# Performance work log

Measured on AMD Instinct MI355X. Metric: run time of the kernel, lower is better.

## Reference

```python
import jax, jax.numpy as jnp
import numpy as np

WS = 5    # window_size
NH = 8    # num_heads
C = 96    # channels
LOG_MAX = float(np.log(1.0 / 0.01))  # clamp max for logit scales


def _conv3x3(x, w, b):
    # NCHW conv, stride 1, padding 1 ('SAME' for 3x3)
    y = jax.lax.conv_general_dilated(x, w, window_strides=(1, 1), padding='SAME',
                                     dimension_numbers=('NCHW', 'OIHW', 'NCHW'))
    return y + b[None, :, None, None]


def _l2norm(x):
    # matches F.normalize(dim=-1): x / max(||x||, 1e-12)
    n = jnp.linalg.norm(x, axis=-1, keepdims=True)
    return x / jnp.maximum(n, 1e-12)


def _wa(f, x, logit_scale):
    # f: (b, c, h, w); x: (b, 2c, h, w) -> windowed cosine attention
    b, c2, h, w = x.shape
    c = f.shape[1]
    hd = c // NH
    H, W = h // WS, w // WS
    # q: b (nh hd) (H ws) (W ws) -> (b H W) nh (ws ws) hd
    q = f.reshape(b, NH, hd, H, WS, W, WS).transpose(0, 3, 5, 1, 4, 6, 2)
    q = q.reshape(b * H * W, NH, WS * WS, hd)
    kv = x.reshape(b, 2, NH, hd, H, WS, W, WS).transpose(1, 0, 4, 6, 2, 5, 7, 3)
    kv = kv.reshape(2, b * H * W, NH, WS * WS, hd)
    k, v = kv[0], kv[1]
    scale = jnp.exp(jnp.minimum(logit_scale, LOG_MAX))  # (NH,1,1)
    atn = jnp.einsum('wnic,wnjc->wnij', _l2norm(q), _l2norm(k)) * scale[None]
    atn = jax.nn.softmax(atn, axis=-1)
    y = jnp.einsum('wnij,wnjc->wnic', atn, v)
    # back to (b, nh*hd, h, w)
    y = y.reshape(b, H, W, NH, WS, WS, hd).transpose(0, 3, 6, 1, 4, 2, 5)
    return y.reshape(b, c, h, w)


def reference(x, w_in, b_in, w_f, b_f, w_out, b_out, logit_scale, lr_logit_scale):
    b, c, h, w = x.shape
    xp = _conv3x3(x, w_in, b_in)   # (b, 2c, h, w)
    fp = _conv3x3(x, w_f, b_f)     # (b, c, h, w)
    sc2, sc = 2 * c // 3, c // 3
    xs = [xp[:, i * sc2:(i + 1) * sc2] for i in range(3)]
    fs = [fp[:, i * sc:(i + 1) * sc] for i in range(3)]
    ys = []
    # branch 0: plain window attention
    ys.append(_wa(fs[0], xs[0], logit_scale))
    # branch 1: shifted windows (torch rolls by -WS//2 = -3 and restores +WS//2 = +2)
    sh = -WS // 2  # Python: (-5)//2 = -3, matches torch code
    x_ = jnp.roll(xs[1], (sh, sh), axis=(2, 3))
    f_ = jnp.roll(fs[1], (sh, sh), axis=(2, 3))
    y_ = _wa(f_, x_, logit_scale)
    ys.append(jnp.roll(y_, (WS // 2, WS // 2), axis=(2, 3)))
    # branch 2: long-range axial (row then column) cosine attention
    hd = sc // NH
    q = fs[2].reshape(b, NH, hd, h, w).transpose(0, 1, 3, 4, 2)            # (b,n,h,w,c)
    kv = xs[2].reshape(b, 2, NH, hd, h, w).transpose(1, 0, 2, 4, 5, 3)      # (2,b,n,h,w,c)
    k, v = kv[0], kv[1]
    qn, kn = _l2norm(q), _l2norm(k)
    scale = jnp.exp(jnp.minimum(lr_logit_scale, LOG_MAX)).reshape(1, NH, 1, 1, 1)
    # row attention (over w)
    atn = jnp.einsum('bnhic,bnhjc->bnhij', qn, kn) * scale
    atn = jax.nn.softmax(atn, axis=-1)
    v = jnp.einsum('bnhij,bnhjc->bnhic', atn, v)
    # column attention (over h), reusing normalized q/k and same scale
    atn = jnp.einsum('bniwc,bnjwc->bnwij', qn, kn) * scale
    atn = jax.nn.softmax(atn, axis=-1)
    v = jnp.einsum('bnwij,bnjwc->bniwc', atn, v)
    ys.append(v.transpose(0, 1, 4, 2, 3).reshape(b, sc, h, w))
    y = jnp.concatenate(ys, axis=1)  # (b, c, h, w)
    return _conv3x3(y, w_out, b_out)


def setup_inputs() -> dict:
    key = jax.random.key(0)
    ks = jax.random.split(key, 8)
    B, H, W = 1, 240, 240
    inp = {
        'x': jax.random.normal(ks[0], (B, C, H, W), dtype=jnp.float32),
        'w_in': jax.random.normal(ks[1], (2 * C, C, 3, 3), dtype=jnp.float32) * 0.03,
        'b_in': jax.random.normal(ks[2], (2 * C,), dtype=jnp.float32) * 0.01,
        'w_f': jax.random.normal(ks[3], (C, C, 3, 3), dtype=jnp.float32) * 0.03,
        'b_f': jax.random.normal(ks[4], (C,), dtype=jnp.float32) * 0.01,
        'w_out': jax.random.normal(ks[5], (C, C, 3, 3), dtype=jnp.float32) * 0.03,
        'b_out': jax.random.normal(ks[6], (C,), dtype=jnp.float32) * 0.01,
        'logit_scale': jnp.log(10.0) * jnp.ones((NH, 1, 1), dtype=jnp.float32),
        'lr_logit_scale': jnp.log(10.0) * jnp.ones((NH, 1, 1), dtype=jnp.float32),
    }
    return inp
```

## Files before the change

### kernel.cpp

```cpp
#include <hip/hip_runtime.h>
#include <math.h>

#define HH 240
#define WW 240
#define PP (HH * WW)
#define PW 242
#define LOG_MAX_C 4.605170185988091f
#define LOG2E 1.442695040888963f

typedef __bf16 bf16x8 __attribute__((ext_vector_type(8)));
typedef float  f32x4  __attribute__((ext_vector_type(4)));

#define EXP2F(x) __builtin_amdgcn_exp2f(x)


__device__ __forceinline__ void to_xs_pad_body(
    int p, const float* __restrict__ in, __bf16* __restrict__ xs)
{
    if (p >= PW * PW) return;
    const int row = p / PW, px = p % PW;
    const bool border = (row == 0 || row == PW - 1 || px == 0 || px == PW - 1);
    union { __bf16 h[32]; uint4 u[4]; } pk;
#pragma unroll
    for (int icb = 0; icb < 3; ++icb) {
        uint4* op = (uint4*)(xs + (((size_t)row * 3 + icb) * PW + px) * 32);
        if (border) {
#pragma unroll
            for (int b = 0; b < 4; ++b) op[b] = make_uint4(0, 0, 0, 0);
        } else {
            const float* ip = in + (size_t)(icb * 32) * PP + (row - 1) * WW + (px - 1);
#pragma unroll
            for (int j = 0; j < 32; ++j) pk.h[j] = (__bf16)ip[(size_t)j * PP];
#pragma unroll
            for (int b = 0; b < 4; ++b) op[b] = pk.u[b];
        }
    }
}

__device__ __forceinline__ void wt_frag_body(
    int t, const float* __restrict__ w, __bf16* __restrict__ wtf, int OC)
{
    if (t >= 9 * (OC / 16) * 3 * 64) return;
    const int lane = t & 63;
    const int rest = t >> 6;
    const int icb  = rest % 3;
    const int to   = rest / 3;
    const int ocb  = to % (OC / 16);
    const int tap  = to / (OC / 16);
    const int ln = lane & 15, quad = lane >> 4;
    const int oc  = ocb * 16 + ln;
    const int ic0 = icb * 32 + quad * 8;
    __bf16* op = wtf + (size_t)rest * 512 + lane * 8;
#pragma unroll
    for (int d = 0; d < 8; ++d)
        op[d] = (__bf16)w[(size_t)(oc * 96 + ic0 + d) * 9 + tap];
}

__global__ __launch_bounds__(256) void prep_kernel(
    const float* __restrict__ x, const float* __restrict__ w_in,
    const float* __restrict__ w_f, const float* __restrict__ w_out,
    __bf16* __restrict__ xs, __bf16* __restrict__ wtf_in,
    __bf16* __restrict__ wtf_f, __bf16* __restrict__ wtf_o)
{
    const int bid = blockIdx.x, tid = threadIdx.x;
    if (bid < 81)       wt_frag_body(bid * 256 + tid, w_in, wtf_in, 192);
    else if (bid < 122) wt_frag_body((bid - 81) * 256 + tid, w_f, wtf_f, 96);
    else if (bid < 163) wt_frag_body((bid - 122) * 256 + tid, w_out, wtf_o, 96);
    else                to_xs_pad_body((bid - 163) * 256 + tid, x, xs);
}

template <int OC, int MT, int EPI>
__device__ __forceinline__ void conv_body(
    int bid, const __bf16* __restrict__ xs, const __bf16* __restrict__ wtf,
    const float* __restrict__ bias, float* __restrict__ out0,
    float* __restrict__ out1, const float* __restrict__ lsc,
    const float* __restrict__ lrlsc, __bf16* As)
{
    const int group = bid / 24;
    const int w24   = bid % 24;
    const int z     = w24 >> 3;
    const int xy    = group * 8 + (w24 & 7);
    if (xy >= 450) return;
    const int x0  = (xy % 15) * 16;
    const int y0  = (xy / 15) * 8;
    const int oc0 = z * (MT * 16);
    const int ocb0 = oc0 / 16;

    const int wave = threadIdx.x >> 6;
    const int lane = threadIdx.x & 63;
    const int ln   = lane & 15;
    const int quad = lane >> 4;
    const int r0   = y0 + wave * 2;

    f32x4 acc[MT][2] = {};
    bf16x8 a[MT], b[2][2], astg;

    const __bf16* abase = wtf + (size_t)lane * 8;
    const __bf16* bbase = xs + (size_t)ln * 32 + quad * 8;

#define ASRC(c) (abase + ((size_t)(((c) / 3) * (OC / 16) + ocb0 + wave) * 3 + (c) % 3) * 512)
#define BLOAD(c, buf)                                                         \
    {                                                                         \
        const int tap_ = (c) / 3, icb_ = (c) % 3;                             \
        const int dy_ = tap_ / 3, dx_ = tap_ % 3;                             \
        _Pragma("unroll")                                                     \
        for (int ni = 0; ni < 2; ++ni)                                        \
            b[buf][ni] = *(const bf16x8*)(bbase +                             \
                (((size_t)(r0 + ni + dy_) * 3 + icb_) * PW + x0 + dx_) * 32); \
    }

    if (wave < MT) {
        astg = *(const bf16x8*)ASRC(0);
        *(bf16x8*)(As + (size_t)wave * 512 + lane * 8) = astg;
        astg = *(const bf16x8*)ASRC(1);
    }
    BLOAD(0, 0)

#pragma unroll
    for (int c = 0; c < 27; ++c) {
        const int cur = c & 1, nxt = cur ^ 1;
        __syncthreads();
        if (c < 26 && wave < MT)
            *(bf16x8*)(As + ((size_t)(nxt * MT) + wave) * 512 + lane * 8) = astg;
#pragma unroll
        for (int mi = 0; mi < MT; ++mi)
            a[mi] = *(const bf16x8*)(As + ((size_t)(cur * MT) + mi) * 512 + lane * 8);
        if (c < 25 && wave < MT)
            astg = *(const bf16x8*)ASRC(c + 2);
        if (c < 26) BLOAD(c + 1, nxt)
#pragma unroll
        for (int mi = 0; mi < MT; ++mi)
#pragma unroll
            for (int ni = 0; ni < 2; ++ni)
                acc[mi][ni] = __builtin_amdgcn_mfma_f32_16x16x32_bf16(
                    a[mi], b[cur][ni], acc[mi][ni], 0, 0, 0);
    }
#undef ASRC
#undef BLOAD

    if constexpr (EPI == 0) {
#pragma unroll
        for (int mi = 0; mi < MT; ++mi) {
#pragma unroll
            for (int r = 0; r < 4; ++r) {
                const int oc = oc0 + mi * 16 + quad * 4 + r;
                const float bv = bias[oc];
#pragma unroll
                for (int ni = 0; ni < 2; ++ni)
                    out0[(size_t)oc * PP + (r0 + ni) * WW + x0 + ln] = acc[mi][ni][r] + bv;
            }
        }
    } else if constexpr (EPI == 1) {
#pragma unroll
        for (int mi = 0; mi < MT; ++mi) {
            const f32x4 bv = *(const f32x4*)(bias + oc0 + mi * 16 + quad * 4);
            float* dst = (mi >> 1) ? out1 : out0;
            const int h8 = z * 8 + (mi & 1) * 4 + quad;
#pragma unroll
            for (int ni = 0; ni < 2; ++ni) {
                f32x4 o = acc[mi][ni] + bv;
                if ((mi >> 1) == 0) {
                    const float ksq = o[0]*o[0] + o[1]*o[1] + o[2]*o[2] + o[3]*o[3];
                    o *= 1.0f / fmaxf(sqrtf(ksq), 1e-12f);
                }
                *(f32x4*)(dst + (((size_t)h8 * 240 + r0 + ni) * 240 + x0 + ln) * 4) = o;
            }
        }
    } else {
#pragma unroll
        for (int mi = 0; mi < MT; ++mi) {
            const f32x4 bv = *(const f32x4*)(bias + oc0 + mi * 16 + quad * 4);
            const int h8 = z * 8 + mi * 4 + quad;
            const int br = h8 >> 3, hh = h8 & 7;
            const float ls = (br == 2) ? lrlsc[hh] : lsc[hh];
            const float qsc = __expf(fminf(ls, LOG_MAX_C)) * LOG2E;
#pragma unroll
            for (int ni = 0; ni < 2; ++ni) {
                f32x4 o = acc[mi][ni] + bv;
                const float qsq = o[0]*o[0] + o[1]*o[1] + o[2]*o[2] + o[3]*o[3];
                o *= qsc / fmaxf(sqrtf(qsq), 1e-12f);
                *(f32x4*)(out0 + (((size_t)h8 * 240 + r0 + ni) * 240 + x0 + ln) * 4) = o;
            }
        }
    }
}

__global__ __launch_bounds__(256) void conv_in_f(
    const __bf16* __restrict__ xs, const __bf16* __restrict__ wtf_in,
    const __bf16* __restrict__ wtf_f, const float* __restrict__ b_in,
    const float* __restrict__ b_f, float* __restrict__ xpk,
    float* __restrict__ xpv, float* __restrict__ fq4,
    const float* __restrict__ lsc, const float* __restrict__ lrlsc)
{
    __shared__ __bf16 As[2 * 4 * 512];
    const int bid = blockIdx.x;
    if (bid < 1368)
        conv_body<192, 4, 1>(bid, xs, wtf_in, b_in, xpk, xpv, nullptr, nullptr, As);
    else
        conv_body<96, 2, 2>(bid - 1368, xs, wtf_f, b_f, fq4, nullptr, lsc, lrlsc, As);
}

__global__ __launch_bounds__(256) void conv_out_k(
    const __bf16* __restrict__ ys, const __bf16* __restrict__ wtf_o,
    const float* __restrict__ b_out, float* __restrict__ out)
{
    __shared__ __bf16 As[2 * 2 * 512];
    conv_body<96, 2, 0>(blockIdx.x, ys, wtf_o, b_out, out, nullptr,
                        nullptr, nullptr, As);
}

__global__ __launch_bounds__(256) void attn_row_fused(
    const float* __restrict__ fq4, const float* __restrict__ xpk,
    const float* __restrict__ xpv, const float* __restrict__ lsc,
    const float* __restrict__ lrlsc, __bf16* __restrict__ ys,
    float* __restrict__ v1)
{
    __shared__ f32x4 sm[960];
    const int bid = blockIdx.x;
    const int t = threadIdx.x;

    if (bid < 960) {
        const int bx = bid >> 3, h = bid & 7;
        const int half = t >> 7, tl = t & 127;
        const int y = bx * 2 + half;
        f32x4* ks = sm;
        f32x4* vs = sm + 480;

        const float scale = __expf(fminf(lrlsc[h], LOG_MAX_C));
        const float negM2 = -scale * LOG2E;
        const size_t rowb = ((size_t)h * 240 + y) * 240;
        const float* fq4b = fq4 + 64 * PP;
        const float* xpkb = xpk + 64 * PP;
        const float* xpvb = xpv + 64 * PP;
        f32x4 qreg[2] = {};

        if (tl < 120) {
#pragma unroll
            for (int s = 0; s < 2; ++s) {
                const int i = tl + s * 120;
                const size_t p4 = (rowb + i) * 4;
                ks[half * 240 + i] = *(const f32x4*)(xpkb + p4);
                vs[half * 240 + i] = *(const f32x4*)(xpvb + p4);
                qreg[s] = *(const f32x4*)(fq4b + p4);
            }
        }
        __syncthreads();
        if (tl < 120) {
            float l0 = 0.f, l1 = 0.f;
            f32x4 a0 = {0, 0, 0, 0}, a1 = {0, 0, 0, 0};
#pragma unroll 4
            for (int j = 0; j < 240; ++j) {
                const f32x4 kk = ks[half * 240 + j];
                const f32x4 vv = vs[half * 240 + j];
                const float s0 = fmaf(qreg[0][0], kk[0],
                                 fmaf(qreg[0][1], kk[1],
                                 fmaf(qreg[0][2], kk[2],
                                 fmaf(qreg[0][3], kk[3], negM2))));
                const float s1 = fmaf(qreg[1][0], kk[0],
                                 fmaf(qreg[1][1], kk[1],
                                 fmaf(qreg[1][2], kk[2],
                                 fmaf(qreg[1][3], kk[3], negM2))));
                const float p0 = EXP2F(s0);
                const float p1 = EXP2F(s1);
                l0 += p0; l1 += p1;
                a0 += vv * p0;
                a1 += vv * p1;
            }
            *(f32x4*)(v1 + (rowb + tl) * 4) = a0 * (1.0f / l0);
            *(f32x4*)(v1 + (rowb + tl + 120) * 4) = a1 * (1.0f / l1);
        }
    } else if (bid < 5568) {
        const int id2 = bid - 960;
        const int br  = id2 / 2304;
        const int id  = id2 % 2304;
        const int wi  = id / 288;
        const int g   = id % 288;
        const int wy  = g / 6;
        const int wx  = (g % 6) * 8 + wi;
        const int gshift = br * 3, sshift = br * 2;
        const size_t choff = (size_t)br * 32 * PP;
        const int h = t / 25, i = t % 25;
        f32x4* ks = sm;
        f32x4* vs = sm + 200;
        f32x4 qn = {0, 0, 0, 0};
        float negM2 = 0.f;
        int oy = 0, ox = 0;

        if (t < 200) {
            const int y = (wy * 5 + i / 5 + gshift) % HH;
            const int x = (wx * 5 + i % 5 + gshift) % WW;
            const size_t p4 = choff + (((size_t)h * 240 + y) * 240 + x) * 4;
            qn = *(const f32x4*)(fq4 + p4);
            ks[h * 25 + i] = *(const f32x4*)(xpk + p4);
            vs[h * 25 + i] = *(const f32x4*)(xpv + p4);
            const float scale = __expf(fminf(lsc[h], LOG_MAX_C));
            negM2 = -scale * LOG2E;
            oy = (wy * 5 + i / 5 + sshift) % HH;
            ox = (wx * 5 + i % 5 + sshift) % WW;
        }
        __syncthreads();
        if (t < 200) {
            float l = 0.f;
            f32x4 acc = {0, 0, 0, 0};
#pragma unroll
            for (int j = 0; j < 25; ++j) {
                const f32x4 kk = ks[h * 25 + j];
                const float s = fmaf(qn[0], kk[0],
                                fmaf(qn[1], kk[1],
                                fmaf(qn[2], kk[2],
                                fmaf(qn[3], kk[3], negM2))));
                const float p = EXP2F(s);
                l += p;
                acc += vs[h * 25 + j] * p;
            }
            const float linv = 1.0f / l;
            union { __bf16 h4[4]; uint2 u; } o;
#pragma unroll
            for (int d = 0; d < 4; ++d) o.h4[d] = (__bf16)(acc[d] * linv);
            *(uint2*)(ys + (((size_t)(oy + 1) * 3 + br) * PW + ox + 1) * 32 + h * 4) = o.u;
        }
    } else {
        const int idx = (bid - 5568) * 256 + t;
        if (idx >= 4 * PW) return;
        const int g = idx / PW, i = idx % PW;
        int row, px;
        if (g == 0)      { row = 0;      px = i; }
        else if (g == 1) { row = PW - 1; px = i; }
        else if (g == 2) { row = i;      px = 0; }
        else             { row = i;      px = PW - 1; }
#pragma unroll
        for (int icb = 0; icb < 3; ++icb) {
            uint4* op = (uint4*)(ys + (((size_t)row * 3 + icb) * PW + px) * 32);
#pragma unroll
            for (int b = 0; b < 4; ++b) op[b] = make_uint4(0, 0, 0, 0);
        }
    }
}

__global__ __launch_bounds__(256) void axial_col_kernel(
    const float* __restrict__ knb, const float* __restrict__ qnb,
    const float* __restrict__ v1b, const float* __restrict__ lsc,
    __bf16* __restrict__ ys)
{
    __shared__ f32x4 ks[2][240];
    __shared__ f32x4 vs[2][240];
    const int bid = blockIdx.x;
    const int wi  = bid / 120;
    const int g   = bid % 120;
    const int h   = g % 8;
    const int xc  = g / 8;
    const int t = threadIdx.x;
    const int half = t >> 7, tl = t & 127;
    const int x = xc * 16 + wi * 2 + half;

    const float scale = __expf(fminf(lsc[h], LOG_MAX_C));
    const float negM2 = -scale * LOG2E;
    const size_t hb = (size_t)h * 240;
    f32x4 qreg[2] = {};

    if (tl < 120) {
#pragma unroll
        for (int s = 0; s < 2; ++s) {
            const int i = tl + s * 120;
            const size_t p4 = ((hb + i) * 240 + x) * 4;
            ks[half][i] = *(const f32x4*)(knb + p4);
            vs[half][i] = *(const f32x4*)(v1b + p4);
            qreg[s] = *(const f32x4*)(qnb + p4);
        }
    }
    __syncthreads();
    if (tl < 120) {
        float l0 = 0.f, l1 = 0.f;
        f32x4 a0 = {0, 0, 0, 0}, a1 = {0, 0, 0, 0};
#pragma unroll 4
        for (int j = 0; j < 240; ++j) {
            const f32x4 kk = ks[half][j];
            const f32x4 vv = vs[half][j];
            const float s0 = fmaf(qreg[0][0], kk[0],
                             fmaf(qreg[0][1], kk[1],
                             fmaf(qreg[0][2], kk[2],
                             fmaf(qreg[0][3], kk[3], negM2))));
            const float s1 = fmaf(qreg[1][0], kk[0],
                             fmaf(qreg[1][1], kk[1],
                             fmaf(qreg[1][2], kk[2],
                             fmaf(qreg[1][3], kk[3], negM2))));
            const float p0 = EXP2F(s0);
            const float p1 = EXP2F(s1);
            l0 += p0; l1 += p1;
            a0 += vv * p0;
            a1 += vv * p1;
        }
#pragma unroll
        for (int s = 0; s < 2; ++s) {
            const f32x4 o4 = s ? a1 * (1.0f / l1) : a0 * (1.0f / l0);
            const int i = tl + s * 120;
            union { __bf16 h4[4]; uint2 u; } o;
#pragma unroll
            for (int d = 0; d < 4; ++d) o.h4[d] = (__bf16)o4[d];
            *(uint2*)(ys + (((size_t)(i + 1) * 3 + 2) * PW + x + 1) * 32 + h * 4) = o.u;
        }
    }
}

extern "C" void kernel_launch(void* const* d_in, const int* in_sizes, int n_in,
                              void* d_out, int out_size, void* d_ws, size_t ws_size,
                              hipStream_t stream)
{
    const float* x     = (const float*)d_in[0];
    const float* w_in  = (const float*)d_in[1];
    const float* b_in  = (const float*)d_in[2];
    const float* w_f   = (const float*)d_in[3];
    const float* b_f   = (const float*)d_in[4];
    const float* w_out = (const float*)d_in[5];
    const float* b_out = (const float*)d_in[6];
    const float* lsc   = (const float*)d_in[7];
    const float* lrlsc = (const float*)d_in[8];
    float* out = (float*)d_out;

    float* ws  = (float*)d_ws;
    float* xpk = ws;
    float* xpv = xpk + 96 * PP;
    float* fq4 = xpv + 96 * PP;
    __bf16* xs     = (__bf16*)(fq4 + 96 * PP);
    __bf16* wtf_in = xs + (size_t)PW * 3 * PW * 32;
    __bf16* wtf_f  = wtf_in + 9 * 12 * 3 * 512;
    __bf16* wtf_o  = wtf_f + 9 * 6 * 3 * 512;
    __bf16* ys     = xs;

    float* v1  = out;

    prep_kernel<<<392, 256, 0, stream>>>(x, w_in, w_f, w_out,
                                         xs, wtf_in, wtf_f, wtf_o);

    conv_in_f<<<2736, 256, 0, stream>>>(xs, wtf_in, wtf_f, b_in, b_f,
                                        xpk, xpv, fq4, lsc, lrlsc);

    attn_row_fused<<<5572, 256, 0, stream>>>(fq4, xpk, xpv, lsc, lrlsc, ys, v1);

    axial_col_kernel<<<960, 256, 0, stream>>>(
        xpk + 64 * PP, fq4 + 64 * PP, v1, lrlsc, ys);

    conv_out_k<<<1368, 256, 0, stream>>>(ys, wtf_o, b_out, out);
}
```

Baseline: 230.9 us.

## Stage conv input halo tile in LDS instead of per-tap global loads

Each conv block now cooperatively copies its 10-row by 18-pixel by 96-channel padded input halo into shared memory once, then reads the B fragments for all 27 tap/channel steps from LDS. This replaces repeated global loads, where the nine taps re-read overlapping pixels, with one bulk load plus cheap LDS reads. It costs about 34 KB of extra LDS per block, which may reduce occupancy. The B prefetch double-buffering is also gone, so LDS read latency now sits on the MFMA path.

```diff
diff --git a/kernel.cpp b/kernel.cpp
--- a/kernel.cpp
+++ b/kernel.cpp
@@ -74,7 +74,7 @@
     int bid, const __bf16* __restrict__ xs, const __bf16* __restrict__ wtf,
     const float* __restrict__ bias, float* __restrict__ out0,
     float* __restrict__ out1, const float* __restrict__ lsc,
-    const float* __restrict__ lrlsc, __bf16* As)
+    const float* __restrict__ lrlsc, __bf16* As, __bf16* Bs)
 {
     const int group = bid / 24;
     const int w24   = bid % 24;
@@ -93,28 +93,34 @@
     const int r0   = y0 + wave * 2;
 
     f32x4 acc[MT][2] = {};
-    bf16x8 a[MT], b[2][2], astg;
+    bf16x8 a[MT], b[2], astg;
 
     const __bf16* abase = wtf + (size_t)lane * 8;
-    const __bf16* bbase = xs + (size_t)ln * 32 + quad * 8;
+
+    {
+        const __bf16* src0 = xs + (size_t)x0 * 32;
+#pragma unroll
+        for (int j = 0; j < 9; ++j) {
+            const int s = j * 256 + threadIdx.x;
+            if (s < 2160) {
+                const int rs = s / 72;
+                const int u  = s % 72;
+                const int px = u >> 2, q = u & 3;
+                const int row = y0 + rs / 3, icb = rs % 3;
+                const uint4 v = *(const uint4*)(src0 +
+                    (((size_t)row * 3 + icb) * PW + px) * 32 + q * 8);
+                *(uint4*)(Bs + (size_t)rs * 576 + px * 32 + q * 8) = v;
+            }
+        }
+    }
 
 #define ASRC(c) (abase + ((size_t)(((c) / 3) * (OC / 16) + ocb0 + wave) * 3 + (c) % 3) * 512)
-#define BLOAD(c, buf)                                                         \
-    {                                                                         \
-        const int tap_ = (c) / 3, icb_ = (c) % 3;                             \
-        const int dy_ = tap_ / 3, dx_ = tap_ % 3;                             \
-        _Pragma("unroll")                                                     \
-        for (int ni = 0; ni < 2; ++ni)                                        \
-            b[buf][ni] = *(const bf16x8*)(bbase +                             \
-                (((size_t)(r0 + ni + dy_) * 3 + icb_) * PW + x0 + dx_) * 32); \
-    }
 
     if (wave < MT) {
         astg = *(const bf16x8*)ASRC(0);
         *(bf16x8*)(As + (size_t)wave * 512 + lane * 8) = astg;
         astg = *(const bf16x8*)ASRC(1);
     }
-    BLOAD(0, 0)
 
 #pragma unroll
     for (int c = 0; c < 27; ++c) {
@@ -125,18 +131,25 @@
 #pragma unroll
         for (int mi = 0; mi < MT; ++mi)
             a[mi] = *(const bf16x8*)(As + ((size_t)(cur * MT) + mi) * 512 + lane * 8);
+        {
+            const int tap_ = c / 3, icb_ = c % 3;
+            const int dy_ = tap_ / 3, dx_ = tap_ % 3;
+#pragma unroll
+            for (int ni = 0; ni < 2; ++ni)
+                b[ni] = *(const bf16x8*)(Bs +
+                    (size_t)((wave * 2 + ni + dy_) * 3 + icb_) * 576 +
+                    (dx_ + ln) * 32 + quad * 8);
+        }
         if (c < 25 && wave < MT)
             astg = *(const bf16x8*)ASRC(c + 2);
-        if (c < 26) BLOAD(c + 1, nxt)
 #pragma unroll
         for (int mi = 0; mi < MT; ++mi)
 #pragma unroll
             for (int ni = 0; ni < 2; ++ni)
                 acc[mi][ni] = __builtin_amdgcn_mfma_f32_16x16x32_bf16(
-                    a[mi], b[cur][ni], acc[mi][ni], 0, 0, 0);
+                    a[mi], b[ni], acc[mi][ni], 0, 0, 0);
     }
 #undef ASRC
-#undef BLOAD
 
     if constexpr (EPI == 0) {
 #pragma unroll
@@ -193,11 +206,14 @@
     const float* __restrict__ lsc, const float* __restrict__ lrlsc)
 {
     __shared__ __bf16 As[2 * 4 * 512];
+    __shared__ __bf16 Bs[30 * 576];
     const int bid = blockIdx.x;
     if (bid < 1368)
-        conv_body<192, 4, 1>(bid, xs, wtf_in, b_in, xpk, xpv, nullptr, nullptr, As);
+        conv_body<192, 4, 1>(bid, xs, wtf_in, b_in, xpk, xpv,
+                             nullptr, nullptr, As, Bs);
     else
-        conv_body<96, 2, 2>(bid - 1368, xs, wtf_f, b_f, fq4, nullptr, lsc, lrlsc, As);
+        conv_body<96, 2, 2>(bid - 1368, xs, wtf_f, b_f, fq4, nullptr,
+                            lsc, lrlsc, As, Bs);
 }
 
 __global__ __launch_bounds__(256) void conv_out_k(
@@ -205,8 +221,9 @@
     const float* __restrict__ b_out, float* __restrict__ out)
 {
     __shared__ __bf16 As[2 * 2 * 512];
+    __shared__ __bf16 Bs[30 * 576];
     conv_body<96, 2, 0>(blockIdx.x, ys, wtf_o, b_out, out, nullptr,
-                        nullptr, nullptr, As);
+                        nullptr, nullptr, As, Bs);
 }
 
 __global__ __launch_bounds__(256) void attn_row_fused(
```

Result: slower. 241.1 us (+4.4%).
